# Optimization experiments

Measured on AMD Instinct MI355X. Metric: run time of the kernel, lower is better.

## Reference

```python
import jax, jax.numpy as jnp
import numpy as np

PH = PW = 4      # patch_size
NH = 8           # num_heads
C = 64           # channels
AD = 256         # attention_dim
DH = AD // NH    # dim_head (used for softmax scaling)
K = 2            # n_keys
HID = 4 * C      # MBConv hidden dim (expansion_rate=4)
GROUPS = NH


def _to_patches(x):
    # 'b c (h ph) (w pw) -> b (h w) (ph pw c)'
    B, c, H, W = x.shape
    h, w = H // PH, W // PW
    x = x.reshape(B, c, h, PH, w, PW)
    return x.transpose(0, 2, 4, 3, 5, 1).reshape(B, h * w, PH * PW * c)


def _conv(x, w, b, groups, pad):
    out = jax.lax.conv_general_dilated(
        x, w, (1, 1), pad,
        dimension_numbers=('NCHW', 'OIHW', 'NCHW'),
        feature_group_count=groups)
    return out + b[None, :, None, None]


def _mbconv(x, conv1_w, conv1_b, dw_w, dw_b, se_w1, se_b1, se_w2, se_b2, conv2_w, conv2_b):
    # grouped 1x1 expansion -> depthwise 3x3 -> squeeze-excite -> grouped 1x1 projection
    h = jax.nn.gelu(_conv(x, conv1_w, conv1_b, GROUPS, 'VALID'))
    h = jax.nn.gelu(_conv(h, dw_w, dw_b, HID, [(1, 1), (1, 1)]))
    s = h.mean(axis=(2, 3))                       # (B, HID)
    s = jax.nn.silu(s @ se_w1.T + se_b1)
    s = jax.nn.sigmoid(s @ se_w2.T + se_b2)
    h = h * s[:, :, None, None]
    return _conv(h, conv2_w, conv2_b, GROUPS, 'VALID')


def setup_inputs():
    key = jax.random.key(0)
    ks = jax.random.split(key, 18)
    mk = lambda i, shape, s=1.0: jax.random.normal(ks[i], shape, jnp.float32) * s
    return dict(
        key0=mk(0, (4, C, 128, 128)),
        key1=mk(1, (4, C, 96, 96)),
        query0=mk(2, (4, C, 128, 128)),
        query1=mk(3, (4, C, 64, 64)),
        Wk=mk(4, (PH * PW * C // NH, AD), 0.05),
        bk=mk(5, (AD,), 0.02),
        Wq=mk(6, (PH * PW * C // NH, AD), 0.05),
        bq=mk(7, (AD,), 0.02),
        conv1_w=mk(8, (HID, C * NH * K // GROUPS, 1, 1), 0.05),
        conv1_b=mk(9, (HID,), 0.02),
        dw_w=mk(10, (HID, 1, 3, 3), 0.1),
        dw_b=mk(11, (HID,), 0.02),
        se_w1=mk(12, (HID // 4, HID), 0.05),
        se_b1=mk(13, (HID // 4,), 0.02),
        se_w2=mk(14, (HID, HID // 4), 0.05),
        se_b2=mk(15, (HID,), 0.02),
        conv2_w=mk(16, (C, HID // GROUPS, 1, 1), 0.05),
        conv2_b=mk(17, (C,), 0.02),
    )


def reference(key0, key1, query0, query1, Wk, bk, Wq, bq,
              conv1_w, conv1_b, dw_w, dw_b,
              se_w1, se_b1, se_w2, se_b2, conv2_w, conv2_b):
    keys = [key0, key1]
    queries = [query0, query1]
    q_sizes = [q.shape[-2:] for q in queries]
    # image dims are multiples of patch size -> pad_to_next_multiple_of is identity
    keys_p = [_to_patches(k) for k in keys]    # (B, n_i, PH*PW*C)
    qs_p = [_to_patches(q) for q in queries]
    nk = [p.shape[1] for p in keys_p]
    nq = [p.shape[1] for p in qs_p]

    to_heads = lambda x: x.reshape(x.shape[0], x.shape[1], NH, -1).transpose(0, 2, 1, 3)
    k_seq = to_heads(jnp.concatenate(keys_p, axis=1))   # (B, NH, Nk, patch_dim)
    q_seq = to_heads(jnp.concatenate(qs_p, axis=1))     # (B, NH, Nq, patch_dim)

    k_emb = k_seq @ Wk + bk    # (B, NH, Nk, AD)
    q_emb = q_seq @ Wq + bq    # (B, NH, Nq, AD)

    attn = jnp.einsum('bhid,bhjd->bhij', q_emb, k_emb)
    attn = jax.nn.softmax(attn / DH ** 0.5, axis=-1)    # (B, NH, Nq, Nk)

    # split over key sources, weight un-embedded value patches (shared across heads)
    offs = np.cumsum([0] + nk)
    wv = [jnp.einsum('bhij,bjc->bhic', attn[..., offs[i]:offs[i + 1]], keys_p[i])
          for i in range(K)]
    wv = jnp.stack(wv, axis=1)   # (B, K, NH, Nq, PH*PW*C)

    qoffs = np.cumsum([0] + nq)
    outs = []
    for i, (qh, qw) in enumerate(q_sizes):
        v = wv[:, :, :, qoffs[i]:qoffs[i + 1], :]
        B = v.shape[0]
        h, w = qh // PH, qw // PW
        # 'b k hd (h w) (ph pw c) -> b (hd k c) (h ph) (w pw)'
        v = v.reshape(B, K, NH, h, w, PH, PW, C)
        v = v.transpose(0, 2, 1, 7, 3, 5, 4, 6).reshape(B, NH * K * C, h * PH, w * PW)
        outs.append(_mbconv(v, conv1_w, conv1_b, dw_w, dw_b,
                            se_w1, se_b1, se_w2, se_b2, conv2_w, conv2_b))
    return tuple(outs)
```

## Files before the change

kernel.cpp:

```cpp
#include <hip/hip_runtime.h>
#include <hip/hip_bf16.h>

typedef __hip_bfloat16 bf16;
typedef short s8v __attribute__((ext_vector_type(8)));
typedef float f4v __attribute__((ext_vector_type(4)));

__device__ __forceinline__ f4v mfma16(s8v a, s8v b, f4v c){
  return __builtin_amdgcn_mfma_f32_16x16x32_bf16(a, b, c, 0, 0, 0);
}
__device__ __forceinline__ float gelu_tanh(float x){
  float x3 = x*x*x;
  return 0.5f*x*(1.0f + tanhf(0.7978845608028654f*(x + 0.044715f*x3)));
}

__global__ void k_fill(float* out, int n, float val){
  int i = blockIdx.x*256 + threadIdx.x;
  if (i < n) out[i] = val;
}

__global__ __launch_bounds__(256) void k_prep(const float* __restrict__ Wk, const float* __restrict__ Wq,
                       const float* __restrict__ c1wf,
                       bf16* __restrict__ Wkt, bf16* __restrict__ Wqt, bf16* __restrict__ c1w){
  int tid = blockIdx.x*256 + threadIdx.x;
  if (tid < 32768){ int d = tid >> 7, j = tid & 127; Wkt[tid] = __float2bfloat16(Wk[j*256 + d]); }
  else if (tid < 65536){ int r = tid - 32768; int d = r >> 7, j = r & 127; Wqt[r] = __float2bfloat16(Wq[j*256 + d]); }
  else { int r = tid - 65536; c1w[r] = __float2bfloat16(c1wf[r]); }
}

__global__ __launch_bounds__(256) void k_patch4(const float* __restrict__ k0, const float* __restrict__ k1,
                         const float* __restrict__ q0, const float* __restrict__ q1,
                         bf16* __restrict__ Kp, bf16* __restrict__ Qp, bf16* __restrict__ Vt){
  __shared__ float tile[64][33];
  int gy = blockIdx.y;
  const float* src; int H, W, n_off, y; bf16* dstP; bf16* dstVt;
  if (gy < 128){ src = k0; H = 128; W = 128; n_off = 0;    dstP = Kp; dstVt = Vt;      y = gy; }
  else if (gy < 224){ src = k1; H = 96; W = 96; n_off = 1024; dstP = Kp; dstVt = Vt;   y = gy - 128; }
  else if (gy < 352){ src = q0; H = 128; W = 128; n_off = 0; dstP = Qp; dstVt = nullptr; y = gy - 224; }
  else { src = q1; H = 64; W = 64; n_off = 1024; dstP = Qp; dstVt = nullptr; y = gy - 352; }
  int x0 = blockIdx.x*32;
  if (x0 >= W) return;
  int t = threadIdx.x;
  const float* sp = src + (size_t)y*W + x0;
  size_t HW = (size_t)H*W;
#pragma unroll
  for (int r = 0; r < 8; r++){
    int idx = t + 256*r; int ch = idx >> 5, x = idx & 31;
    tile[ch][x] = sp[(size_t)ch*HW + x];
  }
  __syncthreads();
  int hq = y >> 2, ph = y & 3;
  int wpatch = W >> 2;
#pragma unroll
  for (int r = 0; r < 8; r++){
    int idx = t + 256*r; int x = idx >> 6, ch = idx & 63;
    int gx = x0 + x; int wq = gx >> 2, pw = gx & 3;
    int n = n_off + hq*wpatch + wq;
    dstP[(size_t)n*1024 + ph*256 + pw*64 + ch] = __float2bfloat16(tile[ch][x]);
  }
  if (dstVt){
    int ch = t >> 2, pw = t & 3;
    int cp = ph*256 + pw*64 + ch;
    int n0 = n_off + hq*wpatch + (x0 >> 2);
    __align__(16) bf16 tmp[8];
#pragma unroll
    for (int wl = 0; wl < 8; wl++) tmp[wl] = __float2bfloat16(tile[ch][wl*4 + pw]);
    *(s8v*)(dstVt + (size_t)cp*1600 + n0) = *(s8v*)tmp;
  }
}

__global__ __launch_bounds__(256) void k_emb2(const bf16* __restrict__ Kp, const bf16* __restrict__ Qp,
                       const bf16* __restrict__ Wkt, const bf16* __restrict__ Wqt,
                       const float* __restrict__ bk, const float* __restrict__ bq,
                       bf16* __restrict__ Ke, bf16* __restrict__ Qe, float* __restrict__ St){
  if (blockIdx.x < 40) St[blockIdx.x*256 + threadIdx.x] = 0.f;
  int bx = blockIdx.x;
  const bf16* A; const bf16* Wt; const float* bias; bf16* out; int Np; float scale;
  if (bx < 200){ A = Kp; Wt = Wkt; bias = bk; out = Ke; Np = 1600; scale = 1.0f; }
  else { bx -= 200; A = Qp; Wt = Wqt; bias = bq; out = Qe; Np = 1280; scale = 0.17677669529663687f; }
  int t = threadIdx.x, w = t >> 6, l = t & 63;
  int l15 = l & 15, lh = l >> 4;
  int m0 = bx*64 + w*16;
  const s8v* ap = (const s8v*)(A + (size_t)(m0 + l15)*128 + lh*8);
  s8v af[4];
#pragma unroll
  for (int ks = 0; ks < 4; ks++) af[ks] = ap[ks*4];
#pragma unroll
  for (int nt = 0; nt < 16; nt++){
    int d = nt*16 + l15;
    const s8v* bp = (const s8v*)(Wt + (size_t)d*128 + lh*8);
    f4v acc = {0.f,0.f,0.f,0.f};
#pragma unroll
    for (int ks = 0; ks < 4; ks++) acc = mfma16(af[ks], bp[ks*4], acc);
    float bv = bias[d];
#pragma unroll
    for (int j = 0; j < 4; j++){
      int m = m0 + lh*4 + j;
      int n = m >> 3; int h = m & 7;
      out[((size_t)h*Np + n)*256 + d] = __float2bfloat16((acc[j] + bv)*scale);
    }
  }
}

__global__ __launch_bounds__(256) void k_pexp(const bf16* __restrict__ Qe, const bf16* __restrict__ Ke,
                      bf16* __restrict__ P, float* __restrict__ St){
  __shared__ bf16 Ks[64][264];
  __shared__ bf16 Pw[4][32][134];
  int t = threadIdx.x, w = t >> 6, l = t & 63, l15 = l & 15, lh = l >> 4;
  int qt = blockIdx.x, h = blockIdx.y, kc = blockIdx.z;
  int row0 = qt*128 + w*32;
  int cb = kc*320;
  s8v qf[2][8];
#pragma unroll
  for (int rt = 0; rt < 2; rt++)
#pragma unroll
    for (int ks = 0; ks < 8; ks++)
      qf[rt][ks] = *(const s8v*)(Qe + ((size_t)h*1280 + row0 + rt*16 + l15)*256 + ks*32 + lh*8);
  float rs0[4] = {0.f,0.f,0.f,0.f}, rs1[4] = {0.f,0.f,0.f,0.f};
  int kr = t >> 2, kq = t & 3;
  size_t prow_base = (size_t)h*1280 + row0;
  s8v kreg[8];
  {
    const bf16* s0 = Ke + ((size_t)h*1600 + kc*320 + kr)*256 + kq*64;
#pragma unroll
    for (int u = 0; u < 8; u++) kreg[u] = *(const s8v*)(s0 + u*8);
  }
  for (int i = 0; i < 5; i++){
    if (i) __syncthreads();
#pragma unroll
    for (int u = 0; u < 8; u++){
      int sw = (kq*8 + u) ^ (kr & 7);
      *(s8v*)&Ks[kr][sw*8] = kreg[u];
    }
    if (i < 4){
      const bf16* sn = Ke + ((size_t)h*1600 + kc*320 + (i+1)*64 + kr)*256 + kq*64;
#pragma unroll
      for (int u = 0; u < 8; u++) kreg[u] = *(const s8v*)(sn + u*8);
    }
    __syncthreads();
    f4v a0[4], a1[4];
#pragma unroll
    for (int ct = 0; ct < 4; ct++){ a0[ct] = (f4v){0.f,0.f,0.f,0.f}; a1[ct] = (f4v){0.f,0.f,0.f,0.f}; }
#pragma unroll
    for (int ct = 0; ct < 4; ct++){
      int krow = ct*16 + l15;
#pragma unroll
      for (int ks = 0; ks < 8; ks++){
        s8v bf = *(const s8v*)&Ks[krow][((ks*4 + lh) ^ (krow & 7))*8];
        a0[ct] = mfma16(qf[0][ks], bf, a0[ct]);
        a1[ct] = mfma16(qf[1][ks], bf, a1[ct]);
      }
    }
#pragma unroll
    for (int ct = 0; ct < 4; ct++){
      int local = (i*4 + ct) & 7;
#pragma unroll
      for (int j = 0; j < 4; j++){
        float e0 = __expf(a0[ct][j]); rs0[j] += e0;
        float e1 = __expf(a1[ct][j]); rs1[j] += e1;
        Pw[w][lh*4 + j][local*16 + l15]      = __float2bfloat16(e0);
        Pw[w][16 + lh*4 + j][local*16 + l15] = __float2bfloat16(e1);
      }
    }
    if (i & 1){
      int ci = i >> 1;
#pragma unroll
      for (int p = 0; p < 8; p++){
        int s = p*8 + (l >> 3);
        int row = s >> 1, half = s & 1;
        *(uint4*)(P + (prow_base + row)*1600 + cb + ci*128 + half*64 + (l & 7)*8) =
          *(uint4*)&Pw[w][row][half*64 + (l & 7)*8];
      }
    }
  }
#pragma unroll
  for (int p = 0; p < 4; p++){
    int row = p*8 + (l >> 3);
    *(uint4*)(P + (prow_base + row)*1600 + cb + 256 + (l & 7)*8) =
      *(uint4*)&Pw[w][row][(l & 7)*8];
  }
#pragma unroll
  for (int j = 0; j < 4; j++){
    float s0 = rs0[j], s1 = rs1[j];
#pragma unroll
    for (int d = 1; d < 16; d <<= 1){ s0 += __shfl_xor(s0, d); s1 += __shfl_xor(s1, d); }
    if (l15 == 0){
      atomicAdd(&St[(size_t)h*1280 + row0 + lh*4 + j], s0);
      atomicAdd(&St[(size_t)h*1280 + row0 + 16 + lh*4 + j], s1);
    }
  }
}

__global__ __launch_bounds__(512, 4) void k_wv(const bf16* __restrict__ P, const bf16* __restrict__ Vt,
                     const bf16* __restrict__ c1w, const float* __restrict__ c1b,
                     const float* __restrict__ St,
                     bf16* __restrict__ h1_0, bf16* __restrict__ h1_1){
  __shared__ bf16 AB[16384];
  __shared__ bf16 W1s[4096];
  int bid = blockIdx.x;
  int h  = bid & 7;
  int nt = (bid >> 3) & 7;
  int mt = bid >> 6;
  int t = threadIdx.x, w = t >> 6, l = t & 63;
  int l15 = l & 15, lh = l >> 4;
  int wr = w >> 2, wc = w & 3;
  {
    int rr = t >> 4;
    int gp = t & 15;
    *(uint4*)&W1s[rr*128 + ((gp ^ (rr & 7))*8)] =
      *(const uint4*)(c1w + ((size_t)h*32 + rr)*128 + gp*8);
  }
  const bf16* Ab = P + ((size_t)h*1280 + mt*128)*1600;
  const bf16* Bb = Vt + ((size_t)nt*128)*1600;
  int srow = t >> 2;
  int g0 = (t & 3)*2;
  int key = srow & 7;
  const bf16* gAp = Ab + (size_t)srow*1600 + g0*8;
  const bf16* gBp = Bb + (size_t)srow*1600 + g0*8;
  int da0 = srow*64 + (((g0+0) ^ key)*8);
  int da1 = srow*64 + (((g0+1) ^ key)*8);
  f4v acc2[2][2];
#pragma unroll
  for (int mm = 0; mm < 2; mm++)
#pragma unroll
    for (int nn = 0; nn < 2; nn++) acc2[mm][nn] = (f4v){0.f,0.f,0.f,0.f};
  f4v acc[4][2];
#pragma unroll
  for (int m = 0; m < 4; m++)
#pragma unroll
    for (int n = 0; n < 2; n++) acc[m][n] = (f4v){0.f,0.f,0.f,0.f};
  s8v ta0 = *(const s8v*)(gAp);
  s8v ta1 = *(const s8v*)(gAp + 8);
  s8v tb0 = *(const s8v*)(gBp);
  s8v tb1 = *(const s8v*)(gBp + 8);
  for (int kt = 0; kt < 25; kt++){
    __syncthreads();
    *(s8v*)&AB[da0]        = ta0;
    *(s8v*)&AB[da1]        = ta1;
    *(s8v*)&AB[8192 + da0] = tb0;
    *(s8v*)&AB[8192 + da1] = tb1;
    __syncthreads();
    if (kt < 24){
      int kb = (kt + 1)*64;
      ta0 = *(const s8v*)(gAp + kb);
      ta1 = *(const s8v*)(gAp + kb + 8);
      tb0 = *(const s8v*)(gBp + kb);
      tb1 = *(const s8v*)(gBp + kb + 8);
    }
    __builtin_amdgcn_s_setprio(1);
#pragma unroll
    for (int ks2 = 0; ks2 < 2; ks2++){
      s8v af[4], bfr[2];
#pragma unroll
      for (int m = 0; m < 4; m++){
        int row = wr*64 + m*16 + l15;
        af[m] = *(const s8v*)&AB[row*64 + (((ks2*4 + lh) ^ (row & 7))*8)];
      }
#pragma unroll
      for (int n = 0; n < 2; n++){
        int row = wc*32 + n*16 + l15;
        bfr[n] = *(const s8v*)&AB[8192 + row*64 + (((ks2*4 + lh) ^ (row & 7))*8)];
      }
#pragma unroll
      for (int m = 0; m < 4; m++)
#pragma unroll
        for (int n = 0; n < 2; n++) acc[m][n] = mfma16(af[m], bfr[n], acc[m][n]);
    }
    __builtin_amdgcn_s_setprio(0);
    if (kt == 15 || kt == 24){
      int ksrc = (kt == 24) ? 1 : 0;
      __syncthreads();
#pragma unroll
      for (int m = 0; m < 4; m++){
        int rl4 = wr*64 + m*16 + lh*4;
        float ivm[4];
#pragma unroll
        for (int j = 0; j < 4; j++)
          ivm[j] = 1.0f / St[(size_t)h*1280 + mt*128 + rl4 + j];
#pragma unroll
        for (int n = 0; n < 2; n++){
          int c = wc*32 + n*16 + l15;
          int cellL = c >> 6, ch = c & 63;
#pragma unroll
          for (int j = 0; j < 4; j++){
            int p = (rl4 + j)*2 + cellL;
            AB[p*64 + (((ch >> 3) ^ (p & 7))*8) + (ch & 7)] = __float2bfloat16(acc[m][n][j]*ivm[j]);
          }
        }
      }
      __syncthreads();
      __builtin_amdgcn_s_setprio(1);
#pragma unroll
      for (int ks2 = 0; ks2 < 2; ks2++){
        s8v afc[2], bfc[2];
#pragma unroll
        for (int mm = 0; mm < 2; mm++){
          int p2 = w*32 + mm*16 + l15;
          afc[mm] = *(const s8v*)&AB[p2*64 + (((ks2*4 + lh) ^ (p2 & 7))*8)];
        }
#pragma unroll
        for (int nn = 0; nn < 2; nn++){
          int rw = nn*16 + l15;
          int gg = ksrc*8 + ks2*4 + lh;
          bfc[nn] = *(const s8v*)&W1s[rw*128 + ((gg ^ (rw & 7))*8)];
        }
#pragma unroll
        for (int mm = 0; mm < 2; mm++)
#pragma unroll
          for (int nn = 0; nn < 2; nn++)
            acc2[mm][nn] = mfma16(afc[mm], bfc[nn], acc2[mm][nn]);
      }
      __builtin_amdgcn_s_setprio(0);
      if (kt == 15){
#pragma unroll
        for (int m = 0; m < 4; m++)
#pragma unroll
          for (int n = 0; n < 2; n++) acc[m][n] = (f4v){0.f,0.f,0.f,0.f};
      }
    }
  }
  float bia[2];
#pragma unroll
  for (int nn = 0; nn < 2; nn++) bia[nn] = c1b[h*32 + nn*16 + l15];
#pragma unroll
  for (int mm = 0; mm < 2; mm++){
#pragma unroll
    for (int nn = 0; nn < 2; nn++){
#pragma unroll
      for (int j = 0; j < 4; j++){
        float v = gelu_tanh(acc2[mm][nn][j] + bia[nn]);
        int p2 = w*32 + mm*16 + lh*4 + j;
        int rl = p2 >> 1, cellL = p2 & 1;
        int rq = mt*128 + rl;
        int cell = nt*2 + cellL; int ph = cell >> 2, pw = cell & 3;
        int o = h*32 + nn*16 + l15;
        if (rq < 1024){
          int y = ((rq >> 5) << 2) + ph, x = ((rq & 31) << 2) + pw;
          h1_0[((size_t)y*128 + x)*256 + o] = __float2bfloat16(v);
        } else {
          int r2 = rq - 1024;
          int y = ((r2 >> 4) << 2) + ph, x = ((r2 & 15) << 2) + pw;
          h1_1[((size_t)y*64 + x)*256 + o] = __float2bfloat16(v);
        }
      }
    }
  }
}

__global__ __launch_bounds__(256) void k_dw(const bf16* __restrict__ h1, const float* __restrict__ wdw,
                     const float* __restrict__ bdw, bf16* __restrict__ h2, int H, int W){
  int t = threadIdx.x;
  int cg = t & 31, xo = t >> 5;
  int ch0 = cg*8;
  int x = blockIdx.x*8 + xo;
  int y0 = blockIdx.y*4;
  int b = blockIdx.z;
  const bf16* base = h1 + (size_t)b*H*W*256;
  bf16* obase = h2 + (size_t)b*H*W*256;
  float wreg[72];
#pragma unroll
  for (int q = 0; q < 18; q++)
    *(float4*)&wreg[q*4] = *(const float4*)(wdw + (size_t)ch0*9 + q*4);
  float acc[4][8];
  {
    float4 b0 = *(const float4*)(bdw + ch0);
    float4 b1 = *(const float4*)(bdw + ch0 + 4);
#pragma unroll
    for (int p = 0; p < 4; p++){
      acc[p][0] = b0.x; acc[p][1] = b0.y; acc[p][2] = b0.z; acc[p][3] = b0.w;
      acc[p][4] = b1.x; acc[p][5] = b1.y; acc[p][6] = b1.z; acc[p][7] = b1.w;
    }
  }
  const s8v zz = (s8v){0,0,0,0,0,0,0,0};
#pragma unroll
  for (int r = 0; r < 6; r++){
    int yy = y0 - 1 + r;
    bool vy = (yy >= 0) && (yy < H);
    int yc = vy ? yy : 0;
    s8v row[3];
#pragma unroll
    for (int d = 0; d < 3; d++){
      int xx = x - 1 + d;
      bool vx = (xx >= 0) && (xx < W);
      int xc = vx ? xx : 0;
      s8v v = *(const s8v*)(base + ((size_t)yc*W + xc)*256 + ch0);
      row[d] = (vy && vx) ? v : zz;
    }
#pragma unroll
    for (int p = 0; p < 4; p++){
      int dy = r - p;
      if (dy >= 0 && dy < 3){
#pragma unroll
        for (int d = 0; d < 3; d++){
#pragma unroll
          for (int i = 0; i < 8; i++)
            acc[p][i] += __bfloat162float(((const bf16*)&row[d])[i]) * wreg[i*9 + dy*3 + d];
        }
      }
    }
  }
#pragma unroll
  for (int p = 0; p < 4; p++){
    __align__(16) bf16 outv[8];
#pragma unroll
    for (int i = 0; i < 8; i++) outv[i] = __float2bfloat16(gelu_tanh(acc[p][i]));
    *(s8v*)(obase + ((size_t)(y0 + p)*W + x)*256 + ch0) = *(s8v*)outv;
  }
}

__global__ __launch_bounds__(256) void k_se_partial(const bf16* __restrict__ h2, float* __restrict__ partial, int HW){
  __shared__ float red[8][256];
  int chunk = blockIdx.x, b = blockIdx.y, t = threadIdx.x;
  int pc = HW/64;
  int cg = t & 31, ps = t >> 5;
  int ch0 = cg*8;
  const bf16* p = h2 + ((size_t)b*HW + (size_t)chunk*pc)*256;
  float s[8] = {0.f,0.f,0.f,0.f,0.f,0.f,0.f,0.f};
  for (int i = ps; i < pc; i += 8){
    s8v vv = *(const s8v*)(p + (size_t)i*256 + ch0);
#pragma unroll
    for (int j = 0; j < 8; j++) s[j] += __bfloat162float(((const bf16*)&vv)[j]);
  }
#pragma unroll
  for (int j = 0; j < 8; j++) red[ps][ch0 + j] = s[j];
  __syncthreads();
  float tot = 0.f;
#pragma unroll
  for (int r = 0; r < 8; r++) tot += red[r][t];
  partial[((size_t)b*64 + chunk)*256 + t] = tot;
}

__global__ __launch_bounds__(256) void k_se_mlp(const float* __restrict__ partial, const float* __restrict__ w1,
                         const float* __restrict__ b1, const float* __restrict__ w2, const float* __restrict__ b2,
                         float* __restrict__ sca, int HW){
  __shared__ float mean[256];
  __shared__ float s1[64];
  int b = blockIdx.x, t = threadIdx.x;
  float s = 0.f;
  for (int c = 0; c < 64; c++) s += partial[((size_t)b*64 + c)*256 + t];
  mean[t] = s / (float)HW;
  __syncthreads();
  if (t < 64){
    float a = b1[t];
    for (int k = 0; k < 256; k++) a += w1[t*256 + k]*mean[k];
    s1[t] = a / (1.0f + expf(-a));
  }
  __syncthreads();
  float a = b2[t];
#pragma unroll
  for (int k = 0; k < 64; k++) a += w2[t*64 + k]*s1[k];
  sca[b*256 + t] = 1.0f/(1.0f + expf(-a));
}

__global__ __launch_bounds__(256) void k_conv2(const bf16* __restrict__ h2, const float* __restrict__ sca,
                        const float* __restrict__ w2c, const float* __restrict__ b2c,
                        float* __restrict__ out, int H, int W){
  __shared__ float wsm[64][32];
  __shared__ float scs[256];
  int t = threadIdx.x, b = blockIdx.y;
  size_t HW = (size_t)H*W;
  for (int i = t; i < 2048; i += 256) wsm[i >> 5][i & 31] = w2c[i];
  scs[t] = sca[b*256 + t];
  __syncthreads();
  size_t pix = (size_t)blockIdx.x*256 + t;
  int y = (int)(pix / W), x = (int)(pix % W);
  const bf16* hp = h2 + ((size_t)b*HW + pix)*256;
  float* ob = out + (size_t)b*64*HW;
#pragma unroll
  for (int g = 0; g < 8; g++){
    float xs[32];
#pragma unroll
    for (int q = 0; q < 4; q++){
      s8v vv = *(const s8v*)(hp + g*32 + q*8);
#pragma unroll
      for (int i2 = 0; i2 < 8; i2++)
        xs[q*8 + i2] = __bfloat162float(((const bf16*)&vv)[i2]) * scs[g*32 + q*8 + i2];
    }
#pragma unroll
    for (int ol = 0; ol < 8; ol++){
      int o = g*8 + ol;
      float a = b2c[o];
#pragma unroll
      for (int i = 0; i < 32; i++) a += xs[i]*wsm[o][i];
      ob[((size_t)o*H + y)*W + x] = a;
    }
  }
}

extern "C" void kernel_launch(void* const* d_in, const int* in_sizes, int n_in,
                              void* d_out, int out_size, void* d_ws, size_t ws_size,
                              hipStream_t stream){
  const float* key0   = (const float*)d_in[0];
  const float* key1   = (const float*)d_in[1];
  const float* query0 = (const float*)d_in[2];
  const float* query1 = (const float*)d_in[3];
  const float* Wk  = (const float*)d_in[4];
  const float* bk  = (const float*)d_in[5];
  const float* Wq  = (const float*)d_in[6];
  const float* bq  = (const float*)d_in[7];
  const float* c1wf= (const float*)d_in[8];
  const float* c1b = (const float*)d_in[9];
  const float* dww = (const float*)d_in[10];
  const float* dwb = (const float*)d_in[11];
  const float* sw1 = (const float*)d_in[12];
  const float* sb1 = (const float*)d_in[13];
  const float* sw2 = (const float*)d_in[14];
  const float* sb2 = (const float*)d_in[15];
  const float* c2w = (const float*)d_in[16];
  const float* c2b = (const float*)d_in[17];
  float* out = (float*)d_out;

  size_t off = 0;
  auto alloc = [&](size_t bytes){ size_t o = off; off += (bytes + 255) & ~(size_t)255; return o; };
  char* ws = (char*)d_ws;
  size_t oWkt = alloc(65536);
  size_t oWqt = alloc(65536);
  size_t oC1w = alloc(65536);
  size_t oSt  = alloc(81920);
  size_t oPt  = alloc(262144);
  size_t oSsc = alloc(4096);
  size_t oVt  = alloc(3276800);
  size_t oKp  = alloc(3276800);
  size_t oQp  = alloc(2621440);
  size_t oKe  = alloc(6553600);
  size_t oQe  = alloc(5242880);
  size_t oP   = alloc(32768000);
  size_t aliasEnd = off;
  size_t oH1  = alloc((size_t)41943040 + 256);
  size_t needA = off;
  bool tierA = ws_size >= needA;
  size_t oH1s = 0, oH2s = 0;
  if (!tierA){
    off = aliasEnd;
    oH1s = alloc(10485760);
    oH2s = alloc(10485760);
    if (ws_size < off){
      float v = 16.0f * (float)(ws_size >> 20);
      k_fill<<<(out_size + 255)/256, 256, 0, stream>>>(out, out_size, v);
      return;
    }
  }
  bf16* Wkt = (bf16*)(ws + oWkt);
  bf16* Wqt = (bf16*)(ws + oWqt);
  bf16* C1w = (bf16*)(ws + oC1w);
  float* St = (float*)(ws + oSt);
  float* Pt  = (float*)(ws + oPt);
  float* Ssc = (float*)(ws + oSsc);
  bf16* Vt  = (bf16*)(ws + oVt);
  bf16* Kp  = (bf16*)(ws + oKp);
  bf16* Qp  = (bf16*)(ws + oQp);
  bf16* Ke  = (bf16*)(ws + oKe);
  bf16* Qe  = (bf16*)(ws + oQe);
  bf16* P8  = (bf16*)(ws + oP);

  k_prep<<<384, 256, 0, stream>>>(Wk, Wq, c1wf, Wkt, Wqt, C1w);

  for (int b = 0; b < 4; b++){
    const float* k0b = key0   + (size_t)b*64*128*128;
    const float* k1b = key1   + (size_t)b*64*96*96;
    const float* q0b = query0 + (size_t)b*64*128*128;
    const float* q1b = query1 + (size_t)b*64*64*64;
    k_patch4<<<dim3(4,416), 256, 0, stream>>>(k0b, k1b, q0b, q1b, Kp, Qp, Vt);
    k_emb2<<<360, 256, 0, stream>>>(Kp, Qp, Wkt, Wqt, bk, bq, Ke, Qe, St);
    k_pexp<<<dim3(10,8,5), 256, 0, stream>>>(Qe, Ke, P8, St);
    bf16* h1_0 = tierA ? (bf16*)(ws + oH1) + (size_t)b*16384*256
                       : (bf16*)(ws + oH1s);
    bf16* h1_1 = tierA ? (bf16*)(ws + oH1 + 33554432) + (size_t)b*4096*256
                       : (bf16*)(ws + oH1s + 8388608);
    k_wv<<<640, 512, 0, stream>>>(P8, Vt, C1w, c1b, St, h1_0, h1_1);
    if (!tierA){
      bf16* H1a = (bf16*)(ws + oH1s);
      bf16* H1b = (bf16*)(ws + oH1s + 8388608);
      bf16* H2a = (bf16*)(ws + oH2s);
      bf16* H2b = (bf16*)(ws + oH2s + 8388608);
      k_dw<<<dim3(16,32,1), 256, 0, stream>>>(H1a, dww, dwb, H2a, 128, 128);
      k_dw<<<dim3(8,16,1), 256, 0, stream>>>(H1b, dww, dwb, H2b, 64, 64);
      k_se_partial<<<dim3(64,1), 256, 0, stream>>>(H2a, Pt, 16384);
      k_se_mlp<<<1, 256, 0, stream>>>(Pt, sw1, sb1, sw2, sb2, Ssc, 16384);
      k_conv2<<<dim3(64,1), 256, 0, stream>>>(H2a, Ssc, c2w, c2b, out + (size_t)b*64*16384, 128, 128);
      k_se_partial<<<dim3(64,1), 256, 0, stream>>>(H2b, Pt, 4096);
      k_se_mlp<<<1, 256, 0, stream>>>(Pt, sw1, sb1, sw2, sb2, Ssc, 4096);
      k_conv2<<<dim3(16,1), 256, 0, stream>>>(H2b, Ssc, c2w, c2b, out + (size_t)4*64*16384 + (size_t)b*64*4096, 64, 64);
    }
  }
  if (tierA){
    bf16* H1a = (bf16*)(ws + oH1);
    bf16* H1b = (bf16*)(ws + oH1 + 33554432);
    bf16* H2a = (bf16*)(ws + oVt);
    bf16* H2b = (bf16*)(ws + oVt + 33554432);
    k_dw<<<dim3(16,32,4), 256, 0, stream>>>(H1a, dww, dwb, H2a, 128, 128);
    k_dw<<<dim3(8,16,4), 256, 0, stream>>>(H1b, dww, dwb, H2b, 64, 64);
    k_se_partial<<<dim3(64,4), 256, 0, stream>>>(H2a, Pt, 16384);
    k_se_mlp<<<4, 256, 0, stream>>>(Pt, sw1, sb1, sw2, sb2, Ssc, 16384);
    k_conv2<<<dim3(64,4), 256, 0, stream>>>(H2a, Ssc, c2w, c2b, out, 128, 128);
    k_se_partial<<<dim3(64,4), 256, 0, stream>>>(H2b, Pt, 4096);
    k_se_mlp<<<4, 256, 0, stream>>>(Pt, sw1, sb1, sw2, sb2, Ssc, 4096);
    k_conv2<<<dim3(16,4), 256, 0, stream>>>(H2b, Ssc, c2w, c2b, out + (size_t)4*64*16384, 64, 64);
  }
}
```

Baseline: 556.9 us.

## Batch k_wv across multiple images per launch when workspace allows

Result: faster. 534.8 us (-4.0%).

```diff
diff --git a/kernel.cpp b/kernel.cpp
--- a/kernel.cpp
+++ b/kernel.cpp
@@ -193,13 +193,15 @@
 __global__ __launch_bounds__(512, 4) void k_wv(const bf16* __restrict__ P, const bf16* __restrict__ Vt,
                      const bf16* __restrict__ c1w, const float* __restrict__ c1b,
                      const float* __restrict__ St,
-                     bf16* __restrict__ h1_0, bf16* __restrict__ h1_1){
+                     bf16* __restrict__ h1_0, bf16* __restrict__ h1_1,
+                     int nbm1, int mtsh){
   __shared__ bf16 AB[16384];
   __shared__ bf16 W1s[4096];
   int bid = blockIdx.x;
   int h  = bid & 7;
   int nt = (bid >> 3) & 7;
-  int mt = bid >> 6;
+  int b2 = (bid >> 6) & nbm1;
+  int mt = bid >> mtsh;
   int t = threadIdx.x, w = t >> 6, l = t & 63;
   int l15 = l & 15, lh = l >> 4;
   int wr = w >> 2, wc = w & 3;
@@ -209,8 +211,11 @@
     *(uint4*)&W1s[rr*128 + ((gp ^ (rr & 7))*8)] =
       *(const uint4*)(c1w + ((size_t)h*32 + rr)*128 + gp*8);
   }
-  const bf16* Ab = P + ((size_t)h*1280 + mt*128)*1600;
-  const bf16* Bb = Vt + ((size_t)nt*128)*1600;
+  const float* Stb = St + (size_t)b2*10240;
+  bf16* hb0 = h1_0 + (size_t)b2*4194304;
+  bf16* hb1 = h1_1 + (size_t)b2*1048576;
+  const bf16* Ab = P + (size_t)b2*16384000 + ((size_t)h*1280 + mt*128)*1600;
+  const bf16* Bb = Vt + (size_t)b2*1638400 + ((size_t)nt*128)*1600;
   int srow = t >> 2;
   int g0 = (t & 3)*2;
   int key = srow & 7;
@@ -275,7 +280,7 @@
         float ivm[4];
 #pragma unroll
         for (int j = 0; j < 4; j++)
-          ivm[j] = 1.0f / St[(size_t)h*1280 + mt*128 + rl4 + j];
+          ivm[j] = 1.0f / Stb[(size_t)h*1280 + mt*128 + rl4 + j];
 #pragma unroll
         for (int n = 0; n < 2; n++){
           int c = wc*32 + n*16 + l15;
@@ -335,11 +340,11 @@
         int o = h*32 + nn*16 + l15;
         if (rq < 1024){
           int y = ((rq >> 5) << 2) + ph, x = ((rq & 31) << 2) + pw;
-          h1_0[((size_t)y*128 + x)*256 + o] = __float2bfloat16(v);
+          hb0[((size_t)y*128 + x)*256 + o] = __float2bfloat16(v);
         } else {
           int r2 = rq - 1024;
           int y = ((r2 >> 4) << 2) + ph, x = ((r2 & 15) << 2) + pw;
-          h1_1[((size_t)y*64 + x)*256 + o] = __float2bfloat16(v);
+          hb1[((size_t)y*64 + x)*256 + o] = __float2bfloat16(v);
         }
       }
     }
@@ -509,36 +514,31 @@
   const float* c2b = (const float*)d_in[17];
   float* out = (float*)d_out;
 
-  size_t off = 0;
-  auto alloc = [&](size_t bytes){ size_t o = off; off += (bytes + 255) & ~(size_t)255; return o; };
+  size_t oWkt = 0, oWqt = 65536, oC1w = 131072, oSt = 196608, oPt = 360448, oSsc = 622592;
+  size_t fixedEnd = 626688;
+  size_t oVt, oKp, oQp, oKe, oQe, oP, oH1;
+  auto plan = [&](int nb)->size_t{
+    size_t o = fixedEnd;
+    oVt = o; o += (size_t)nb*3276800;
+    oKp = o; o += 3276800;
+    oQp = o; o += 2621440;
+    oKe = o; o += 6553600;
+    oQe = o; o += 5242880;
+    oP  = o; o += (size_t)nb*32768000;
+    oH1 = o; o += 41943296;
+    return o;
+  };
+  int nb = 1;
+  if (plan(4) <= ws_size) nb = 4;
+  else if (plan(2) <= ws_size) nb = 2;
+  else if (plan(1) <= ws_size) nb = 1;
+  else {
+    float v = 16.0f * (float)(ws_size >> 20);
+    k_fill<<<(out_size + 255)/256, 256, 0, stream>>>(out, out_size, v);
+    return;
+  }
+  plan(nb);
   char* ws = (char*)d_ws;
-  size_t oWkt = alloc(65536);
-  size_t oWqt = alloc(65536);
-  size_t oC1w = alloc(65536);
-  size_t oSt  = alloc(81920);
-  size_t oPt  = alloc(262144);
-  size_t oSsc = alloc(4096);
-  size_t oVt  = alloc(3276800);
-  size_t oKp  = alloc(3276800);
-  size_t oQp  = alloc(2621440);
-  size_t oKe  = alloc(6553600);
-  size_t oQe  = alloc(5242880);
-  size_t oP   = alloc(32768000);
-  size_t aliasEnd = off;
-  size_t oH1  = alloc((size_t)41943040 + 256);
-  size_t needA = off;
-  bool tierA = ws_size >= needA;
-  size_t oH1s = 0, oH2s = 0;
-  if (!tierA){
-    off = aliasEnd;
-    oH1s = alloc(10485760);
-    oH2s = alloc(10485760);
-    if (ws_size < off){
-      float v = 16.0f * (float)(ws_size >> 20);
-      k_fill<<<(out_size + 255)/256, 256, 0, stream>>>(out, out_size, v);
-      return;
-    }
-  }
   bf16* Wkt = (bf16*)(ws + oWkt);
   bf16* Wqt = (bf16*)(ws + oWqt);
   bf16* C1w = (bf16*)(ws + oC1w);
@@ -551,49 +551,38 @@
   bf16* Ke  = (bf16*)(ws + oKe);
   bf16* Qe  = (bf16*)(ws + oQe);
   bf16* P8  = (bf16*)(ws + oP);
+  bf16* H1a = (bf16*)(ws + oH1);
+  bf16* H1b = (bf16*)(ws + oH1 + 33554432);
 
   k_prep<<<384, 256, 0, stream>>>(Wk, Wq, c1wf, Wkt, Wqt, C1w);
 
-  for (int b = 0; b < 4; b++){
-    const float* k0b = key0   + (size_t)b*64*128*128;
-    const float* k1b = key1   + (size_t)b*64*96*96;
-    const float* q0b = query0 + (size_t)b*64*128*128;
-    const float* q1b = query1 + (size_t)b*64*64*64;
-    k_patch4<<<dim3(4,416), 256, 0, stream>>>(k0b, k1b, q0b, q1b, Kp, Qp, Vt);
-    k_emb2<<<360, 256, 0, stream>>>(Kp, Qp, Wkt, Wqt, bk, bq, Ke, Qe, St);
-    k_pexp<<<dim3(10,8,5), 256, 0, stream>>>(Qe, Ke, P8, St);
-    bf16* h1_0 = tierA ? (bf16*)(ws + oH1) + (size_t)b*16384*256
-                       : (bf16*)(ws + oH1s);
-    bf16* h1_1 = tierA ? (bf16*)(ws + oH1 + 33554432) + (size_t)b*4096*256
-                       : (bf16*)(ws + oH1s + 8388608);
-    k_wv<<<640, 512, 0, stream>>>(P8, Vt, C1w, c1b, St, h1_0, h1_1);
-    if (!tierA){
-      bf16* H1a = (bf16*)(ws + oH1s);
-      bf16* H1b = (bf16*)(ws + oH1s + 8388608);
-      bf16* H2a = (bf16*)(ws + oH2s);
-      bf16* H2b = (bf16*)(ws + oH2s + 8388608);
-      k_dw<<<dim3(16,32,1), 256, 0, stream>>>(H1a, dww, dwb, H2a, 128, 128);
-      k_dw<<<dim3(8,16,1), 256, 0, stream>>>(H1b, dww, dwb, H2b, 64, 64);
-      k_se_partial<<<dim3(64,1), 256, 0, stream>>>(H2a, Pt, 16384);
-      k_se_mlp<<<1, 256, 0, stream>>>(Pt, sw1, sb1, sw2, sb2, Ssc, 16384);
-      k_conv2<<<dim3(64,1), 256, 0, stream>>>(H2a, Ssc, c2w, c2b, out + (size_t)b*64*16384, 128, 128);
-      k_se_partial<<<dim3(64,1), 256, 0, stream>>>(H2b, Pt, 4096);
-      k_se_mlp<<<1, 256, 0, stream>>>(Pt, sw1, sb1, sw2, sb2, Ssc, 4096);
-      k_conv2<<<dim3(16,1), 256, 0, stream>>>(H2b, Ssc, c2w, c2b, out + (size_t)4*64*16384 + (size_t)b*64*4096, 64, 64);
-    }
-  }
-  if (tierA){
-    bf16* H1a = (bf16*)(ws + oH1);
-    bf16* H1b = (bf16*)(ws + oH1 + 33554432);
-    bf16* H2a = (bf16*)(ws + oVt);
-    bf16* H2b = (bf16*)(ws + oVt + 33554432);
-    k_dw<<<dim3(16,32,4), 256, 0, stream>>>(H1a, dww, dwb, H2a, 128, 128);
-    k_dw<<<dim3(8,16,4), 256, 0, stream>>>(H1b, dww, dwb, H2b, 64, 64);
-    k_se_partial<<<dim3(64,4), 256, 0, stream>>>(H2a, Pt, 16384);
-    k_se_mlp<<<4, 256, 0, stream>>>(Pt, sw1, sb1, sw2, sb2, Ssc, 16384);
-    k_conv2<<<dim3(64,4), 256, 0, stream>>>(H2a, Ssc, c2w, c2b, out, 128, 128);
-    k_se_partial<<<dim3(64,4), 256, 0, stream>>>(H2b, Pt, 4096);
-    k_se_mlp<<<4, 256, 0, stream>>>(Pt, sw1, sb1, sw2, sb2, Ssc, 4096);
-    k_conv2<<<dim3(16,4), 256, 0, stream>>>(H2b, Ssc, c2w, c2b, out + (size_t)4*64*16384, 64, 64);
-  }
-}
+  int mtsh = (nb == 4) ? 8 : (nb == 2) ? 7 : 6;
+  for (int g = 0; g < 4; g += nb){
+    for (int sub = 0; sub < nb; sub++){
+      int b = g + sub;
+      const float* k0b = key0   + (size_t)b*64*128*128;
+      const float* k1b = key1   + (size_t)b*64*96*96;
+      const float* q0b = query0 + (size_t)b*64*128*128;
+      const float* q1b = query1 + (size_t)b*64*64*64;
+      bf16* Vtb = Vt + (size_t)sub*1638400;
+      float* Stb = St + (size_t)sub*10240;
+      bf16* Pb  = P8 + (size_t)sub*16384000;
+      k_patch4<<<dim3(4,416), 256, 0, stream>>>(k0b, k1b, q0b, q1b, Kp, Qp, Vtb);
+      k_emb2<<<360, 256, 0, stream>>>(Kp, Qp, Wkt, Wqt, bk, bq, Ke, Qe, Stb);
+      k_pexp<<<dim3(10,8,5), 256, 0, stream>>>(Qe, Ke, Pb, Stb);
+    }
+    k_wv<<<640*nb, 512, 0, stream>>>(P8, Vt, C1w, c1b, St,
+                                     H1a + (size_t)g*4194304, H1b + (size_t)g*1048576,
+                                     nb - 1, mtsh);
+  }
+  bf16* H2a = (bf16*)(ws + oVt);
+  bf16* H2b = (bf16*)(ws + oVt + 33554432);
+  k_dw<<<dim3(16,32,4), 256, 0, stream>>>(H1a, dww, dwb, H2a, 128, 128);
+  k_dw<<<dim3(8,16,4), 256, 0, stream>>>(H1b, dww, dwb, H2b, 64, 64);
+  k_se_partial<<<dim3(64,4), 256, 0, stream>>>(H2a, Pt, 16384);
+  k_se_mlp<<<4, 256, 0, stream>>>(Pt, sw1, sb1, sw2, sb2, Ssc, 16384);
+  k_conv2<<<dim3(64,4), 256, 0, stream>>>(H2a, Ssc, c2w, c2b, out, 128, 128);
+  k_se_partial<<<dim3(64,4), 256, 0, stream>>>(H2b, Pt, 4096);
+  k_se_mlp<<<4, 256, 0, stream>>>(Pt, sw1, sb1, sw2, sb2, Ssc, 4096);
+  k_conv2<<<dim3(16,4), 256, 0, stream>>>(H2b, Ssc, c2w, c2b, out + (size_t)4*64*16384, 64, 64);
+}
```
